# Kernel optimization log

Hardware: AMD Instinct MI355X
Metric: run time of the kernel (lower is better)

## Reference

```python
import jax, jax.numpy as jnp
import numpy as np

EPS = 1e-06


def setup_inputs() -> dict:
    key = jax.random.key(0)
    k1, k2 = jax.random.split(key)
    N, C, H, W = 32, 4, 512, 512
    inp = jax.random.normal(k1, (N, C, H, W), dtype=jnp.float32)
    target = jax.random.randint(k2, (N, 1, H, W), 0, C, dtype=jnp.int32)
    return {"input": inp, "target": target}


def reference(input, target):
    # softmax over class dim
    probs = jax.nn.softmax(input, axis=1)  # [N, C, H, W]
    # intersection = sum_{c,h,w} probs * one_hot(target)
    # == sum_{h,w} probs gathered at the target class (avoids one-hot materialization)
    gathered = jnp.take_along_axis(probs, target.astype(jnp.int32), axis=1)  # [N,1,H,W]
    intersection = jnp.sum(gathered, axis=(1, 2, 3))  # [N]
    # cardinality = sum probs + sum one_hot; one-hot sums to 1 per pixel -> H*W per sample
    hw = jnp.asarray(input.shape[2] * input.shape[3], dtype=probs.dtype)
    cardinality = jnp.sum(probs, axis=(1, 2, 3)) + hw  # [N]
    dice_score = 2.0 * intersection / (cardinality + EPS)
    return jnp.mean(1.0 - dice_score)
```

## Files before the change

### kernel.cpp

```cpp
#include <hip/hip_runtime.h>


constexpr int N_   = 32;
constexpr int C_   = 4;
constexpr int HW_  = 512 * 512;
constexpr float EPSF = 1e-6f;

__global__ __launch_bounds__(256) void dice_partial(
        const float* __restrict__ x,
        const int*   __restrict__ tgt,
        float*       __restrict__ partial,
        int ngroups) {
    int tid    = blockIdx.x * blockDim.x + threadIdx.x;
    int stride = gridDim.x * blockDim.x;
    float acc = 0.f;

    for (int g = tid; g < ngroups; g += stride) {
        int pix = g << 2;
        int n   = pix >> 18;
        int hw  = pix & (HW_ - 1);
        const float* base = x + (size_t)n * C_ * HW_ + hw;

        float4 v0 = *reinterpret_cast<const float4*>(base);
        float4 v1 = *reinterpret_cast<const float4*>(base + HW_);
        float4 v2 = *reinterpret_cast<const float4*>(base + 2 * (size_t)HW_);
        float4 v3 = *reinterpret_cast<const float4*>(base + 3 * (size_t)HW_);
        int4   t4 = *reinterpret_cast<const int4*>(tgt + (size_t)n * HW_ + hw);

        const float* a0 = reinterpret_cast<const float*>(&v0);
        const float* a1 = reinterpret_cast<const float*>(&v1);
        const float* a2 = reinterpret_cast<const float*>(&v2);
        const float* a3 = reinterpret_cast<const float*>(&v3);
        const int*   tt = reinterpret_cast<const int*>(&t4);

        #pragma unroll
        for (int j = 0; j < 4; ++j) {
            float a = a0[j], b = a1[j], c = a2[j], d = a3[j];
            int   t = tt[j];
            float m  = fmaxf(fmaxf(a, b), fmaxf(c, d));
            float ea = __expf(a - m);
            float eb = __expf(b - m);
            float ec = __expf(c - m);
            float ed = __expf(d - m);
            float denom = (ea + eb) + (ec + ed);
            float et = (t == 0) ? ea : (t == 1) ? eb : (t == 2) ? ec : ed;
            acc += et / denom;
        }
    }

    #pragma unroll
    for (int off = 32; off > 0; off >>= 1)
        acc += __shfl_down(acc, off, 64);

    __shared__ float wsum[4];
    int lane = threadIdx.x & 63;
    int wid  = threadIdx.x >> 6;
    if (lane == 0) wsum[wid] = acc;
    __syncthreads();
    if (threadIdx.x == 0)
        partial[blockIdx.x] = (wsum[0] + wsum[1]) + (wsum[2] + wsum[3]);
}

__global__ __launch_bounds__(256) void dice_final(
        const float* __restrict__ partial, int nblk, float* __restrict__ out) {
    float acc = 0.f;
    for (int i = threadIdx.x; i < nblk; i += blockDim.x)
        acc += partial[i];

    #pragma unroll
    for (int off = 32; off > 0; off >>= 1)
        acc += __shfl_down(acc, off, 64);

    __shared__ float wsum[4];
    int lane = threadIdx.x & 63;
    int wid  = threadIdx.x >> 6;
    if (lane == 0) wsum[wid] = acc;
    __syncthreads();
    if (threadIdx.x == 0) {
        float S    = (wsum[0] + wsum[1]) + (wsum[2] + wsum[3]);
        float card = 2.0f * (float)HW_ + EPSF;
        out[0] = 1.0f - 2.0f * S / ((float)N_ * card);
    }
}

extern "C" void kernel_launch(void* const* d_in, const int* in_sizes, int n_in,
                              void* d_out, int out_size, void* d_ws, size_t ws_size,
                              hipStream_t stream) {
    const float* x   = (const float*)d_in[0];
    const int*   tgt = (const int*)d_in[1];
    float*       out = (float*)d_out;
    float*       par = (float*)d_ws;

    int nblk = 2048;
    if (ws_size < (size_t)nblk * sizeof(float))
        nblk = (int)(ws_size / sizeof(float));
    if (nblk < 1) nblk = 1;

    constexpr int ngroups = N_ * HW_ / 4;

    dice_partial<<<nblk, 256, 0, stream>>>(x, tgt, par, ngroups);
    dice_final<<<1, 256, 0, stream>>>(par, nblk, out);
}
```

Measured before the change: 34.43 us.

## Fuse final reduction via last-block ticket and batch all loads upfront

Merges the partial and final reduction kernels into one launch: each block publishes its partial sum and increments a global ticket, and the last block performs the final reduction. It also fixes the geometry at compile time so each thread issues all its loads (NITER iterations of 4 channels plus target) before any compute, raising memory-level parallelism. This removes a second kernel launch but adds a memset, atomics and higher register pressure from holding all loaded vectors.

```diff
diff --git a/kernel.cpp b/kernel.cpp
--- a/kernel.cpp
+++ b/kernel.cpp
@@ -6,37 +6,45 @@
 constexpr int HW_  = 512 * 512;
 constexpr float EPSF = 1e-6f;
 
-__global__ __launch_bounds__(256) void dice_partial(
+constexpr int NBLK  = 2048;
+constexpr int NTHR  = 256;
+constexpr int TOTTH = NBLK * NTHR;
+constexpr int NGROUPS = N_ * HW_ / 4;
+constexpr int NITER = NGROUPS / TOTTH;
+static_assert(NITER * TOTTH == NGROUPS, "geometry must tile exactly");
+
+__global__ __launch_bounds__(NTHR) void dice_fused(
         const float* __restrict__ x,
         const int*   __restrict__ tgt,
         float*       __restrict__ partial,
-        int ngroups) {
-    int tid    = blockIdx.x * blockDim.x + threadIdx.x;
-    int stride = gridDim.x * blockDim.x;
+        unsigned*    __restrict__ ticket,
+        float*       __restrict__ out) {
+    const int tid = blockIdx.x * NTHR + threadIdx.x;
+
+    float4 v[NITER][C_];
+    int4   t4[NITER];
+    #pragma unroll
+    for (int it = 0; it < NITER; ++it) {
+        const int pix = (tid + it * TOTTH) << 2;
+        const int n   = pix >> 18;
+        const int hw  = pix & (HW_ - 1);
+        const float* base = x + (size_t)n * (C_ * HW_) + hw;
+        #pragma unroll
+        for (int c = 0; c < C_; ++c)
+            v[it][c] = *reinterpret_cast<const float4*>(base + (size_t)c * HW_);
+        t4[it] = *reinterpret_cast<const int4*>(tgt + (size_t)n * HW_ + hw);
+    }
+
     float acc = 0.f;
-
-    for (int g = tid; g < ngroups; g += stride) {
-        int pix = g << 2;
-        int n   = pix >> 18;
-        int hw  = pix & (HW_ - 1);
-        const float* base = x + (size_t)n * C_ * HW_ + hw;
-
-        float4 v0 = *reinterpret_cast<const float4*>(base);
-        float4 v1 = *reinterpret_cast<const float4*>(base + HW_);
-        float4 v2 = *reinterpret_cast<const float4*>(base + 2 * (size_t)HW_);
-        float4 v3 = *reinterpret_cast<const float4*>(base + 3 * (size_t)HW_);
-        int4   t4 = *reinterpret_cast<const int4*>(tgt + (size_t)n * HW_ + hw);
-
-        const float* a0 = reinterpret_cast<const float*>(&v0);
-        const float* a1 = reinterpret_cast<const float*>(&v1);
-        const float* a2 = reinterpret_cast<const float*>(&v2);
-        const float* a3 = reinterpret_cast<const float*>(&v3);
-        const int*   tt = reinterpret_cast<const int*>(&t4);
-
+    #pragma unroll
+    for (int it = 0; it < NITER; ++it) {
         #pragma unroll
         for (int j = 0; j < 4; ++j) {
-            float a = a0[j], b = a1[j], c = a2[j], d = a3[j];
-            int   t = tt[j];
+            float a = reinterpret_cast<const float*>(&v[it][0])[j];
+            float b = reinterpret_cast<const float*>(&v[it][1])[j];
+            float c = reinterpret_cast<const float*>(&v[it][2])[j];
+            float d = reinterpret_cast<const float*>(&v[it][3])[j];
+            int   t = reinterpret_cast<const int*>(&t4[it])[j];
             float m  = fmaxf(fmaxf(a, b), fmaxf(c, d));
             float ea = __expf(a - m);
             float eb = __expf(b - m);
@@ -52,34 +60,42 @@
     for (int off = 32; off > 0; off >>= 1)
         acc += __shfl_down(acc, off, 64);
 
-    __shared__ float wsum[4];
-    int lane = threadIdx.x & 63;
-    int wid  = threadIdx.x >> 6;
+    __shared__ float wsum[NTHR / 64];
+    __shared__ int   lastFlag;
+    const int lane = threadIdx.x & 63;
+    const int wid  = threadIdx.x >> 6;
     if (lane == 0) wsum[wid] = acc;
     __syncthreads();
-    if (threadIdx.x == 0)
-        partial[blockIdx.x] = (wsum[0] + wsum[1]) + (wsum[2] + wsum[3]);
-}
 
-__global__ __launch_bounds__(256) void dice_final(
-        const float* __restrict__ partial, int nblk, float* __restrict__ out) {
-    float acc = 0.f;
-    for (int i = threadIdx.x; i < nblk; i += blockDim.x)
-        acc += partial[i];
+    if (threadIdx.x == 0) {
+        float bs = (wsum[0] + wsum[1]) + (wsum[2] + wsum[3]);
+        atomicExch(reinterpret_cast<unsigned*>(&partial[blockIdx.x]),
+                   __float_as_uint(bs));
+        __threadfence();
+        unsigned old = atomicAdd(ticket, 1u);
+        lastFlag = (old == (unsigned)(NBLK - 1));
+    }
+    __syncthreads();
 
-    #pragma unroll
-    for (int off = 32; off > 0; off >>= 1)
-        acc += __shfl_down(acc, off, 64);
-
-    __shared__ float wsum[4];
-    int lane = threadIdx.x & 63;
-    int wid  = threadIdx.x >> 6;
-    if (lane == 0) wsum[wid] = acc;
-    __syncthreads();
-    if (threadIdx.x == 0) {
-        float S    = (wsum[0] + wsum[1]) + (wsum[2] + wsum[3]);
-        float card = 2.0f * (float)HW_ + EPSF;
-        out[0] = 1.0f - 2.0f * S / ((float)N_ * card);
+    if (lastFlag) {
+        __threadfence();
+        float a = 0.f;
+        #pragma unroll
+        for (int r = 0; r < NBLK / NTHR; ++r) {
+            int i = r * NTHR + threadIdx.x;
+            a += __uint_as_float(
+                atomicAdd(reinterpret_cast<unsigned*>(&partial[i]), 0u));
+        }
+        #pragma unroll
+        for (int off = 32; off > 0; off >>= 1)
+            a += __shfl_down(a, off, 64);
+        if (lane == 0) wsum[wid] = a;
+        __syncthreads();
+        if (threadIdx.x == 0) {
+            float S    = (wsum[0] + wsum[1]) + (wsum[2] + wsum[3]);
+            float card = 2.0f * (float)HW_ + EPSF;
+            out[0] = 1.0f - 2.0f * S / ((float)N_ * card);
+        }
     }
 }
 
@@ -89,15 +105,11 @@
     const float* x   = (const float*)d_in[0];
     const int*   tgt = (const int*)d_in[1];
     float*       out = (float*)d_out;
-    float*       par = (float*)d_ws;
 
-    int nblk = 2048;
-    if (ws_size < (size_t)nblk * sizeof(float))
-        nblk = (int)(ws_size / sizeof(float));
-    if (nblk < 1) nblk = 1;
+    float*    partial = (float*)d_ws;
+    unsigned* ticket  = (unsigned*)((char*)d_ws + (size_t)NBLK * sizeof(float));
 
-    constexpr int ngroups = N_ * HW_ / 4;
+    hipMemsetAsync(ticket, 0, sizeof(unsigned), stream);
 
-    dice_partial<<<nblk, 256, 0, stream>>>(x, tgt, par, ngroups);
-    dice_final<<<1, 256, 0, stream>>>(par, nblk, out);
+    dice_fused<<<NBLK, NTHR, 0, stream>>>(x, tgt, partial, ticket, out);
 }
```

After: 99.20 us. +188.1%, slower.
